# Optimization experiments

Hardware: AMD Instinct MI355X
Metric: run time of the kernel (lower is better)

The kernel has to match this reference:

```python
import jax, jax.numpy as jnp
import numpy as np

NUM_INPUTS = 512
NUM_CENTROIDS = 4096
BATCH = 16384


def setup_inputs() -> dict:
    key = jax.random.key(0)
    k_x, k_a, k_g, k_b, k_z = jax.random.split(key, 5)
    X = jax.random.normal(k_x, (BATCH, NUM_INPUTS), dtype=jnp.float32)
    # parameter init mirrors RBFN.initialize()
    alpha = jax.random.uniform(k_a, (1,), minval=-2.0, maxval=2.0, dtype=jnp.float32)
    log_gamma = jax.random.uniform(
        k_g, (1,),
        minval=-0.1 - np.log(NUM_INPUTS), maxval=0.1 - np.log(NUM_INPUTS),
        dtype=jnp.float32)
    beta = jax.random.uniform(k_b, (NUM_CENTROIDS,), minval=-2.0, maxval=2.0, dtype=jnp.float32)
    Z = jax.random.uniform(k_z, (NUM_INPUTS, NUM_CENTROIDS), minval=-2.0, maxval=2.0, dtype=jnp.float32)
    return {"X": X, "alpha": alpha, "log_gamma": log_gamma, "beta": beta, "Z": Z}


def reference(X, alpha, log_gamma, beta, Z):
    # B = X @ Z : [batch, num_centroids]
    B = jnp.dot(X, Z)
    x_sq = jnp.sum(X * X, axis=1, keepdims=True)          # [batch, 1]
    z_sq = jnp.sum(Z * Z, axis=0)                          # [num_centroids]
    D = x_sq + z_sq - 2.0 * B                              # [batch, num_centroids]
    gamma = jnp.exp(log_gamma)                             # [1]
    A = jnp.exp(-gamma * D)                                # RBF activations
    pred = alpha + A @ beta                                # [batch]
    return pred
```

## Files before the change

kernel.cpp:

```cpp
#include <hip/hip_runtime.h>
#include <hip/hip_bf16.h>

#define MM 16384
#define NN 4096
#define KK 512

typedef __bf16 bf16x8 __attribute__((ext_vector_type(8)));
typedef float  f32x4  __attribute__((ext_vector_type(4)));

__global__ __launch_bounds__(256) void prep_x_kernel(
    const float* __restrict__ X, const float* __restrict__ alpha,
    __bf16* __restrict__ Xb, float* __restrict__ x_sq, float* __restrict__ out)
{
    int row  = blockIdx.x * 4 + (threadIdx.x >> 6);
    int lane = threadIdx.x & 63;
    const float4* src = (const float4*)(X + (size_t)row * KK) + lane * 2;
    float4 a = src[0];
    float4 b = src[1];
    float s = a.x*a.x + a.y*a.y + a.z*a.z + a.w*a.w
            + b.x*b.x + b.y*b.y + b.z*b.z + b.w*b.w;
    bf16x8 v;
    v[0]=(__bf16)a.x; v[1]=(__bf16)a.y; v[2]=(__bf16)a.z; v[3]=(__bf16)a.w;
    v[4]=(__bf16)b.x; v[5]=(__bf16)b.y; v[6]=(__bf16)b.z; v[7]=(__bf16)b.w;
    *(bf16x8*)(Xb + (size_t)row * KK + lane * 8) = v;
    #pragma unroll
    for (int o = 1; o < 64; o <<= 1) s += __shfl_xor(s, o);
    if (lane == 0) { x_sq[row] = s; out[row] = alpha[0]; }
}

__global__ __launch_bounds__(256) void prep_zt_kernel(
    const float* __restrict__ Z, __bf16* __restrict__ Zt, float* __restrict__ z_sq)
{
    __shared__ float t[64][65];
    const int n0 = blockIdx.x * 64;
    const int k0 = blockIdx.y * 64;
    const int tid = threadIdx.x;
    const int j = tid & 63, i0 = tid >> 6;
    #pragma unroll
    for (int p = 0; p < 16; ++p) {
        int i = i0 * 16 + p;
        t[i][j] = Z[(size_t)(k0 + i) * NN + n0 + j];
    }
    __syncthreads();
    const int nl = tid >> 2, kc = tid & 3;
    bf16x8 v0, v1;
    float s = 0.0f;
    #pragma unroll
    for (int e = 0; e < 8; ++e) {
        float x = t[kc * 16 + e][nl];
        v0[e] = (__bf16)x; s += x * x;
    }
    #pragma unroll
    for (int e = 0; e < 8; ++e) {
        float x = t[kc * 16 + 8 + e][nl];
        v1[e] = (__bf16)x; s += x * x;
    }
    __bf16* dst = Zt + (size_t)(n0 + nl) * KK + k0 + kc * 16;
    *(bf16x8*)(dst)     = v0;
    *(bf16x8*)(dst + 8) = v1;
    s += __shfl_xor(s, 1);
    s += __shfl_xor(s, 2);
    if (kc == 0) atomicAdd(&z_sq[n0 + nl], s);
}

__global__ __launch_bounds__(512, 2) void rbfn_kernel(
    const __bf16* __restrict__ Xb, const __bf16* __restrict__ Zt,
    const float* __restrict__ x_sq, const float* __restrict__ z_sq,
    const float* __restrict__ beta, const float* __restrict__ log_gamma,
    float* __restrict__ out)
{
    __shared__ __bf16 As[3][256 * 32];
    __shared__ __bf16 Bs[3][256 * 32];

    const int tid  = threadIdx.x;
    const int wid  = tid >> 6;
    const int lane = tid & 63;
    const int wr   = wid >> 2;
    const int wcn  = wid & 3;
    const int row0 = blockIdx.x * 256;
    const int col0 = blockIdx.y * 256;

    const int srow = lane >> 2;
    const int skel = (((lane & 3) ^ ((lane >> 3) & 3)) * 8);
    const __bf16* Ab = Xb + (size_t)(row0 + wid * 32 + srow) * KK + skel;
    const __bf16* Bb = Zt + (size_t)(col0 + wid * 32 + srow) * KK + skel;

#define GLDS(gp, lp) __builtin_amdgcn_global_load_lds( \
        (const __attribute__((address_space(1))) void*)(gp), \
        (__attribute__((address_space(3))) void*)(lp), 16, 0, 0)
#define STAGE_A(kt, b) do { const size_t _ko = (size_t)(kt) * 32; \
        GLDS(Ab + _ko,           &As[b][wid * 1024]); \
        GLDS(Ab + 16*KK + _ko,   &As[b][wid * 1024 + 512]); } while (0)
#define STAGE_B(kt, b) do { const size_t _ko = (size_t)(kt) * 32; \
        GLDS(Bb + _ko,           &Bs[b][wid * 1024]); \
        GLDS(Bb + 16*KK + _ko,   &Bs[b][wid * 1024 + 512]); } while (0)

    f32x4 acc[8][4] = {};

    STAGE_A(0, 0); STAGE_B(0, 0);
    STAGE_A(1, 1); STAGE_B(1, 1);
    asm volatile("s_waitcnt vmcnt(4)" ::: "memory");
    __builtin_amdgcn_s_barrier();

    const int l15 = lane & 15;
    const int gcol = lane >> 4;

    int cur = 0;
    #pragma unroll 1
    for (int t = 0; t < 16; ++t) {
        const int sb = (cur >= 1) ? cur - 1 : cur + 2;
        const bool stage_ok = (t + 2 < 16);
        const char* curA = (const char*)As[cur];
        const char* curB = (const char*)Bs[cur];

        bf16x8 af[4], bfv[4];

        #pragma unroll
        for (int m = 0; m < 4; ++m) {
            const int rr = wr * 128 + m * 16 + l15;
            const int off = rr * 64 + (((gcol ^ ((rr >> 1) & 3))) << 4);
            af[m] = *(const bf16x8*)(curA + off);
        }
        #pragma unroll
        for (int n = 0; n < 4; ++n) {
            const int rb = wcn * 64 + n * 16 + l15;
            const int off = rb * 64 + (((gcol ^ ((rb >> 1) & 3))) << 4);
            bfv[n] = *(const bf16x8*)(curB + off);
        }
        if (stage_ok) STAGE_A(t + 2, sb);
        __builtin_amdgcn_s_barrier();
        asm volatile("s_waitcnt lgkmcnt(0)" ::: "memory");
        __builtin_amdgcn_sched_barrier(0);
        __builtin_amdgcn_s_setprio(1);
        #pragma unroll
        for (int m = 0; m < 4; ++m)
            #pragma unroll
            for (int n = 0; n < 4; ++n)
                acc[m][n] = __builtin_amdgcn_mfma_f32_16x16x32_bf16(
                    af[m], bfv[n], acc[m][n], 0, 0, 0);
        __builtin_amdgcn_s_setprio(0);
        __builtin_amdgcn_s_barrier();

        #pragma unroll
        for (int m = 0; m < 4; ++m) {
            const int rr = wr * 128 + (m + 4) * 16 + l15;
            const int off = rr * 64 + (((gcol ^ ((rr >> 1) & 3))) << 4);
            af[m] = *(const bf16x8*)(curA + off);
        }
        if (stage_ok) STAGE_B(t + 2, sb);
        __builtin_amdgcn_s_barrier();
        asm volatile("s_waitcnt lgkmcnt(0)" ::: "memory");
        __builtin_amdgcn_sched_barrier(0);
        __builtin_amdgcn_s_setprio(1);
        #pragma unroll
        for (int m = 0; m < 4; ++m)
            #pragma unroll
            for (int n = 0; n < 4; ++n)
                acc[m + 4][n] = __builtin_amdgcn_mfma_f32_16x16x32_bf16(
                    af[m], bfv[n], acc[m + 4][n], 0, 0, 0);
        __builtin_amdgcn_s_setprio(0);

        if (t <= 13)       asm volatile("s_waitcnt vmcnt(4)" ::: "memory");
        else if (t == 14)  asm volatile("s_waitcnt vmcnt(0)" ::: "memory");
        __builtin_amdgcn_s_barrier();

        cur = (cur >= 2) ? 0 : cur + 1;
    }
#undef STAGE_A
#undef STAGE_B
#undef GLDS

    const float gamma = __expf(log_gamma[0]);
    const float c2    = gamma * 1.4426950408889634f;
    const float twoc2 = 2.0f * c2;

    float czn[4], bet[4];
    const int colb = col0 + wcn * 64 + l15;
    #pragma unroll
    for (int n = 0; n < 4; ++n) {
        const int c = colb + n * 16;
        czn[n] = -c2 * z_sq[c];
        bet[n] = beta[c];
    }

    const int rowb = row0 + wr * 128 + (lane >> 4) * 4;
    #pragma unroll
    for (int m = 0; m < 8; ++m) {
        #pragma unroll
        for (int j = 0; j < 4; ++j) {
            const int r = rowb + m * 16 + j;
            const float cx = -c2 * x_sq[r];
            float p = 0.0f;
            #pragma unroll
            for (int n = 0; n < 4; ++n) {
                const float arg = fmaf(twoc2, acc[m][n][j], cx + czn[n]);
                p = fmaf(exp2f(arg), bet[n], p);
            }
            p += __shfl_xor(p, 1);
            p += __shfl_xor(p, 2);
            p += __shfl_xor(p, 4);
            p += __shfl_xor(p, 8);
            if (l15 == 0) atomicAdd(&out[r], p);
        }
    }
}

extern "C" void kernel_launch(void* const* d_in, const int* in_sizes, int n_in,
                              void* d_out, int out_size, void* d_ws, size_t ws_size,
                              hipStream_t stream) {
    const float* X         = (const float*)d_in[0];
    const float* alpha     = (const float*)d_in[1];
    const float* log_gamma = (const float*)d_in[2];
    const float* beta      = (const float*)d_in[3];
    const float* Z         = (const float*)d_in[4];

    char* ws = (char*)d_ws;
    __bf16* Xb   = (__bf16*)(ws);
    __bf16* Zt   = (__bf16*)(ws + 16777216);
    float*  x_sq = (float*) (ws + 20971520);
    float*  z_sq = (float*) (ws + 21037056);
    float*  out  = (float*)d_out;

    hipMemsetAsync(z_sq, 0, NN * sizeof(float), stream);
    prep_x_kernel <<<4096, 256, 0, stream>>>(X, alpha, Xb, x_sq, out);
    prep_zt_kernel<<<dim3(64, 8), 256, 0, stream>>>(Z, Zt, z_sq);
    rbfn_kernel   <<<dim3(64, 16), 512, 0, stream>>>(Xb, Zt, x_sq, z_sq, beta, log_gamma, out);
}
```

Measured before the change: 220.8 us.

## Replace atomics with deterministic partial-sum reductions and swizzle block order

The z_sq atomics are replaced by per-k-block partial sums, and the memset is removed. The output atomics are replaced by an LDS cross-wave reduction that writes per-column-tile partials, which a new reduce kernel sums together with alpha. The change also remaps blockIdx.x for better L2 locality, relaxes launch_bounds occupancy, and removes explicit lgkmcnt waits and sched barriers before the MFMAs. Together these aim to cut atomic traffic and launch overhead, at the cost of an extra kernel and partial-buffer traffic, and they rely on the compiler to insert the correct waits.

New measurement: 187.7 us. 15.0% less time.

```diff
diff --git a/kernel.cpp b/kernel.cpp
--- a/kernel.cpp
+++ b/kernel.cpp
@@ -9,8 +9,8 @@
 typedef float  f32x4  __attribute__((ext_vector_type(4)));
 
 __global__ __launch_bounds__(256) void prep_x_kernel(
-    const float* __restrict__ X, const float* __restrict__ alpha,
-    __bf16* __restrict__ Xb, float* __restrict__ x_sq, float* __restrict__ out)
+    const float* __restrict__ X,
+    __bf16* __restrict__ Xb, float* __restrict__ x_sq)
 {
     int row  = blockIdx.x * 4 + (threadIdx.x >> 6);
     int lane = threadIdx.x & 63;
@@ -25,11 +25,12 @@
     *(bf16x8*)(Xb + (size_t)row * KK + lane * 8) = v;
     #pragma unroll
     for (int o = 1; o < 64; o <<= 1) s += __shfl_xor(s, o);
-    if (lane == 0) { x_sq[row] = s; out[row] = alpha[0]; }
+    if (lane == 0) x_sq[row] = s;
 }
 
 __global__ __launch_bounds__(256) void prep_zt_kernel(
-    const float* __restrict__ Z, __bf16* __restrict__ Zt, float* __restrict__ z_sq)
+    const float* __restrict__ Z, __bf16* __restrict__ Zt,
+    float* __restrict__ zsq_part)
 {
     __shared__ float t[64][65];
     const int n0 = blockIdx.x * 64;
@@ -60,14 +61,14 @@
     *(bf16x8*)(dst + 8) = v1;
     s += __shfl_xor(s, 1);
     s += __shfl_xor(s, 2);
-    if (kc == 0) atomicAdd(&z_sq[n0 + nl], s);
-}
-
-__global__ __launch_bounds__(512, 2) void rbfn_kernel(
+    if (kc == 0) zsq_part[blockIdx.y * NN + n0 + nl] = s;
+}
+
+__global__ __launch_bounds__(512) void rbfn_kernel(
     const __bf16* __restrict__ Xb, const __bf16* __restrict__ Zt,
-    const float* __restrict__ x_sq, const float* __restrict__ z_sq,
+    const float* __restrict__ x_sq, const float* __restrict__ zsq_part,
     const float* __restrict__ beta, const float* __restrict__ log_gamma,
-    float* __restrict__ out)
+    float* __restrict__ partial)
 {
     __shared__ __bf16 As[3][256 * 32];
     __shared__ __bf16 Bs[3][256 * 32];
@@ -77,8 +78,11 @@
     const int lane = tid & 63;
     const int wr   = wid >> 2;
     const int wcn  = wid & 3;
-    const int row0 = blockIdx.x * 256;
-    const int col0 = blockIdx.y * 256;
+    const int bx   = blockIdx.x;
+    const int cxt  = (bx & 7) * 8 + (bx >> 3);
+    const int cy   = blockIdx.y;
+    const int row0 = cxt * 256;
+    const int col0 = cy * 256;
 
     const int srow = lane >> 2;
     const int skel = (((lane & 3) ^ ((lane >> 3) & 3)) * 8);
@@ -129,8 +133,6 @@
         }
         if (stage_ok) STAGE_A(t + 2, sb);
         __builtin_amdgcn_s_barrier();
-        asm volatile("s_waitcnt lgkmcnt(0)" ::: "memory");
-        __builtin_amdgcn_sched_barrier(0);
         __builtin_amdgcn_s_setprio(1);
         #pragma unroll
         for (int m = 0; m < 4; ++m)
@@ -149,8 +151,6 @@
         }
         if (stage_ok) STAGE_B(t + 2, sb);
         __builtin_amdgcn_s_barrier();
-        asm volatile("s_waitcnt lgkmcnt(0)" ::: "memory");
-        __builtin_amdgcn_sched_barrier(0);
         __builtin_amdgcn_s_setprio(1);
         #pragma unroll
         for (int m = 0; m < 4; ++m)
@@ -179,17 +179,21 @@
     #pragma unroll
     for (int n = 0; n < 4; ++n) {
         const int c = colb + n * 16;
-        czn[n] = -c2 * z_sq[c];
+        float zs = 0.0f;
+        #pragma unroll
+        for (int q = 0; q < 8; ++q) zs += zsq_part[q * NN + c];
+        czn[n] = -c2 * zs;
         bet[n] = beta[c];
     }
 
-    const int rowb = row0 + wr * 128 + (lane >> 4) * 4;
+    float* red = (float*)&As[0][0];
+    const int g4 = lane >> 4;
     #pragma unroll
     for (int m = 0; m < 8; ++m) {
         #pragma unroll
         for (int j = 0; j < 4; ++j) {
-            const int r = rowb + m * 16 + j;
-            const float cx = -c2 * x_sq[r];
+            const int rloc = m * 16 + g4 * 4 + j;
+            const float cx = -c2 * x_sq[row0 + wr * 128 + rloc];
             float p = 0.0f;
             #pragma unroll
             for (int n = 0; n < 4; ++n) {
@@ -200,9 +204,27 @@
             p += __shfl_xor(p, 2);
             p += __shfl_xor(p, 4);
             p += __shfl_xor(p, 8);
-            if (l15 == 0) atomicAdd(&out[r], p);
-        }
-    }
+            if (l15 == 0) red[(wr * 4 + wcn) * 128 + rloc] = p;
+        }
+    }
+    __syncthreads();
+    if (tid < 256) {
+        const int w = tid >> 7, rloc = tid & 127;
+        float s = red[(w * 4 + 0) * 128 + rloc] + red[(w * 4 + 1) * 128 + rloc]
+                + red[(w * 4 + 2) * 128 + rloc] + red[(w * 4 + 3) * 128 + rloc];
+        partial[(size_t)cy * MM + row0 + tid] = s;
+    }
+}
+
+__global__ __launch_bounds__(256) void reduce_kernel(
+    const float* __restrict__ partial, const float* __restrict__ alpha,
+    float* __restrict__ out)
+{
+    const int r = blockIdx.x * 256 + threadIdx.x;
+    float s = alpha[0];
+    #pragma unroll
+    for (int q = 0; q < 16; ++q) s += partial[(size_t)q * MM + r];
+    out[r] = s;
 }
 
 extern "C" void kernel_launch(void* const* d_in, const int* in_sizes, int n_in,
@@ -215,14 +237,16 @@
     const float* Z         = (const float*)d_in[4];
 
     char* ws = (char*)d_ws;
-    __bf16* Xb   = (__bf16*)(ws);
-    __bf16* Zt   = (__bf16*)(ws + 16777216);
-    float*  x_sq = (float*) (ws + 20971520);
-    float*  z_sq = (float*) (ws + 21037056);
-    float*  out  = (float*)d_out;
-
-    hipMemsetAsync(z_sq, 0, NN * sizeof(float), stream);
-    prep_x_kernel <<<4096, 256, 0, stream>>>(X, alpha, Xb, x_sq, out);
-    prep_zt_kernel<<<dim3(64, 8), 256, 0, stream>>>(Z, Zt, z_sq);
-    rbfn_kernel   <<<dim3(64, 16), 512, 0, stream>>>(Xb, Zt, x_sq, z_sq, beta, log_gamma, out);
-}
+    __bf16* Xb       = (__bf16*)(ws);
+    __bf16* Zt       = (__bf16*)(ws + 16777216);
+    float*  x_sq     = (float*) (ws + 20971520);
+    float*  zsq_part = (float*) (ws + 21037056);
+    float*  partial  = (float*) (ws + 21168128);
+    float*  out      = (float*)d_out;
+
+    prep_x_kernel <<<4096, 256, 0, stream>>>(X, Xb, x_sq);
+    prep_zt_kernel<<<dim3(64, 8), 256, 0, stream>>>(Z, Zt, zsq_part);
+    rbfn_kernel   <<<dim3(64, 16), 512, 0, stream>>>(Xb, Zt, x_sq, zsq_part,
+                                                     beta, log_gamma, partial);
+    reduce_kernel <<<64, 256, 0, stream>>>(partial, alpha, out);
+}
```
